# Kernel optimization log

Measured on AMD Instinct MI355X. Metric: run time of the kernel, lower is better.

Reference implementation:

```python
import jax, jax.numpy as jnp
import numpy as np

N, B, D = 4, 256, 128  # agents, batch, latent dim; hidden = 2*D


def setup_inputs() -> dict:
    key = jax.random.key(0)
    k1, k2, k3, k4, k5 = jax.random.split(key, 5)
    z_all = jax.random.normal(k1, (N, B, D), dtype=jnp.float32)
    # per-agent MLP params, stacked over agents; torch Linear layout [out, in]
    W1 = jax.random.normal(k2, (N, 2 * D, D), dtype=jnp.float32) * 0.08
    b1 = jax.random.normal(k3, (N, 2 * D), dtype=jnp.float32) * 0.05
    W2 = jax.random.normal(k4, (N, 1, 2 * D), dtype=jnp.float32) * 0.06
    b2 = jax.random.normal(k5, (N, 1), dtype=jnp.float32) * 0.05
    return {"z_all": z_all, "W1": W1, "b1": b1, "W2": W2, "b2": b2}


def _value(z, W1i, b1i, W2i, b2i):
    # V_i(z): Linear(D,2D) -> tanh -> Linear(2D,1), squeezed to scalar
    h = jnp.tanh(W1i @ z + b1i)          # [2D]
    return jnp.dot(W2i[0], h) + b2i[0]   # scalar


def _pair_hessian(zb, W1i, b1i, W2i, b2i):
    # Hessian of V_i w.r.t. z, batched over B -> [B, D, D]
    hess = jax.hessian(lambda z: _value(z, W1i, b1i, W2i, b2i))
    return jax.vmap(hess)(zb)


def reference(z_all, W1, b1, W2, b2):
    Bn, Dn = z_all.shape[1], z_all.shape[2]
    zero = jnp.zeros((Bn, Dn, Dn), dtype=z_all.dtype)
    rows = []
    for i in range(N):
        cols = []
        for j in range(N):
            if i == j:
                cols.append(zero)
            else:
                cols.append(_pair_hessian(z_all[j], W1[i], b1[i], W2[i], b2[i]))
        rows.append(jnp.stack(cols, axis=0))
    return jnp.stack(rows, axis=0)  # [N, N, B, D, D]
```

## Files before the change

### kernel.cpp

```cpp
#include <hip/hip_runtime.h>
#include <hip/hip_bf16.h>

#define NA 4
#define BB 256
#define DDm 128
#define KKm 256

typedef __attribute__((ext_vector_type(4))) float f32x4;
typedef __attribute__((ext_vector_type(4))) unsigned int u32x4;
typedef __attribute__((ext_vector_type(8))) short bf16x8;

__device__ __forceinline__ unsigned int f2bf(float f) {
  unsigned int bits = __builtin_bit_cast(unsigned int, f);
  unsigned int lsb = (bits >> 16) & 1u;
  return (bits + 0x7fffu + lsb) >> 16;
}

__device__ __forceinline__ int swz_off(int a, int k2bytes) {
  return ((a << 9) + k2bytes) ^ ((a & 7) << 4);
}

__global__ __launch_bounds__(256) void prep_kernel(const float* __restrict__ W1,
                                                   unsigned short* __restrict__ Wt_g,
                                                   float* __restrict__ W1T) {
  int blk = blockIdx.x;
  int i = blk >> 3;
  int chunk = blk & 7;
  const float* W1i = W1 + i * KKm * DDm;
  char* Wti = (char*)(Wt_g + i * 32768);
  float* W1Ti = W1T + i * DDm * KKm;
  int base = chunk * 4096;
  for (int idx = base + threadIdx.x; idx < base + 4096; idx += 256) {
    int a = idx >> 8;
    int k = idx & 255;
    float v = W1i[k * DDm + a];
    W1Ti[a * KKm + k] = v;
    *(unsigned short*)(Wti + swz_off(a, k << 1)) = (unsigned short)f2bf(v);
  }
}

__global__ __launch_bounds__(256, 2) void hess_kernel(
    const float* __restrict__ z_all, const float* __restrict__ b1,
    const float* __restrict__ W2, const unsigned short* __restrict__ Wt_g,
    const float* __restrict__ W1T, float* __restrict__ out) {
  __shared__ __align__(16) unsigned short Wt[32768];
  __shared__ __align__(16) float s_lds[8][KKm];

  int t = threadIdx.x;
  int blk = blockIdx.x;
  int pair = blk >> 5;
  int bgrp = blk & 31;
  int i = pair >> 2;
  int j = pair & 3;

  if (i == j) {
    f32x4* zp = (f32x4*)(out + (((size_t)pair * BB + bgrp * 8) << 14));
    f32x4 z4 = (f32x4){0.f, 0.f, 0.f, 0.f};
#pragma unroll
    for (int q = 0; q < 128; ++q) zp[q * 256 + t] = z4;
    return;
  }

  {
    int wv = t >> 6, lane = t & 63;
    const char* src = (const char*)(Wt_g + i * 32768);
#pragma unroll
    for (int it = 0; it < 16; ++it) {
      int off = (it * 4 + wv) * 1024;
      __builtin_amdgcn_global_load_lds(
          (const __attribute__((address_space(1))) unsigned int*)(src + off + lane * 16),
          (__attribute__((address_space(3))) unsigned int*)((char*)Wt + off),
          16, 0, 0);
    }
  }

  {
    const float* w = W1T + i * DDm * KKm + t;
    const float* zj = z_all + ((size_t)j * BB + bgrp * 8) * DDm;
    float ub = b1[i * KKm + t];
    float u[8];
#pragma unroll
    for (int v = 0; v < 8; ++v) u[v] = ub;
#pragma unroll 4
    for (int a = 0; a < DDm; ++a) {
      float wa = w[a * KKm];
#pragma unroll
      for (int v = 0; v < 8; ++v) u[v] = fmaf(wa, zj[v * DDm + a], u[v]);
    }
    float w2v = W2[i * KKm + t];
#pragma unroll
    for (int v = 0; v < 8; ++v) {
      float h = tanhf(u[v]);
      s_lds[v][t] = -2.0f * w2v * h * (1.0f - h * h);
    }
  }
  __syncthreads();

  int wvi = t >> 6, lane = t & 63;
  int g = lane >> 4;
  int lr = lane & 15;
  int bset = wvi >> 1;
  int rb0 = (wvi & 1) * 64;

  f32x4 accA[2][8], accB[2][8];

  auto do_chunk = [&](f32x4 (&acc)[2][8], int rowbase, const float* sb, float* op) {
#pragma unroll
    for (int mt = 0; mt < 2; ++mt)
#pragma unroll
      for (int nt = 0; nt < 8; ++nt) acc[mt][nt] = (f32x4){0.f, 0.f, 0.f, 0.f};

    for (int kc = 0; kc < 8; ++kc) {
      int kbyte = kc * 64 + g * 16;
      const f32x4* sp = (const f32x4*)&sb[kc * 32 + g * 8];
      f32x4 sA = sp[0], sB = sp[1];
      float sv[8] = {sA[0], sA[1], sA[2], sA[3], sB[0], sB[1], sB[2], sB[3]};

      bf16x8 afr[2];
#pragma unroll
      for (int mt = 0; mt < 2; ++mt) {
        int row = rowbase + mt * 16 + lr;
        u32x4 wq = *(const u32x4*)((const char*)Wt + swz_off(row, kbyte));
        u32x4 aq;
#pragma unroll
        for (int q = 0; q < 4; ++q) {
          float lo = __builtin_bit_cast(float, wq[q] << 16) * sv[2 * q];
          float hi = __builtin_bit_cast(float, wq[q] & 0xffff0000u) * sv[2 * q + 1];
          unsigned int lb = __builtin_bit_cast(unsigned short, (__bf16)lo);
          unsigned int hb = __builtin_bit_cast(unsigned short, (__bf16)hi);
          aq[q] = lb | (hb << 16);
        }
        afr[mt] = __builtin_bit_cast(bf16x8, aq);
      }

#pragma unroll
      for (int nt = 0; nt < 8; ++nt) {
        int row = nt * 16 + lr;
        bf16x8 bfr = __builtin_bit_cast(
            bf16x8, *(const u32x4*)((const char*)Wt + swz_off(row, kbyte)));
        acc[0][nt] = __builtin_amdgcn_mfma_f32_16x16x32_bf16(afr[0], bfr, acc[0][nt], 0, 0, 0);
        acc[1][nt] = __builtin_amdgcn_mfma_f32_16x16x32_bf16(afr[1], bfr, acc[1][nt], 0, 0, 0);
      }
    }

#pragma unroll
    for (int mt = 0; mt < 2; ++mt) {
      int rbase = rowbase + mt * 16 + g * 4;
#pragma unroll
      for (int nt = 0; nt < 8; ++nt) {
        int col = nt * 16 + lr;
#pragma unroll
        for (int q = 0; q < 4; ++q) op[(size_t)(rbase + q) * DDm + col] = acc[mt][nt][q];
      }
    }
  };

  for (int bb = 0; bb < 4; ++bb) {
    int bloc = bset * 4 + bb;
    const float* sb = &s_lds[bloc][0];
    float* op = out + (((size_t)pair * BB + bgrp * 8 + bloc) << 14);
    do_chunk(accA, rb0, sb, op);
    do_chunk(accB, rb0 + 32, sb, op);
  }
}

extern "C" void kernel_launch(void* const* d_in, const int* in_sizes, int n_in,
                              void* d_out, int out_size, void* d_ws, size_t ws_size,
                              hipStream_t stream) {
  const float* z_all = (const float*)d_in[0];
  const float* W1 = (const float*)d_in[1];
  const float* b1 = (const float*)d_in[2];
  const float* W2 = (const float*)d_in[3];
  float* out = (float*)d_out;

  unsigned short* Wt_g = (unsigned short*)d_ws;
  float* W1T = (float*)((char*)d_ws + 262144);

  prep_kernel<<<32, 256, 0, stream>>>(W1, Wt_g, W1T);
  hess_kernel<<<16 * 32, 256, 0, stream>>>(z_all, b1, W2, Wt_g, W1T, out);
}
```

Baseline: 69.12 us.

## Overlap previous chunk's global stores with current chunk's MFMA loop

Software-pipelines the Hessian output writes. The stores of the previous 32-row accumulator set are interleaved into the k-loop of the next chunk, and the k-loop is fully unrolled, so global write traffic overlaps with MFMA and LDS work instead of being serialized after each chunk. Keeping two live accumulator sets adds register pressure, and stores are spread one column tile per k-step.

```diff
diff --git a/kernel.cpp b/kernel.cpp
--- a/kernel.cpp
+++ b/kernel.cpp
@@ -100,16 +100,19 @@
   int g = lane >> 4;
   int lr = lane & 15;
   int bset = wvi >> 1;
-  int rb0 = (wvi & 1) * 64;
+  int m0 = (wvi & 1) * 64;
 
   f32x4 accA[2][8], accB[2][8];
 
-  auto do_chunk = [&](f32x4 (&acc)[2][8], int rowbase, const float* sb, float* op) {
+  auto run_chunk = [&](f32x4 (&acc)[2][8], int rowbase, const float* sb,
+                       bool hasPrev, f32x4 (&pacc)[2][8], int prowbase,
+                       float* pop) {
 #pragma unroll
     for (int mt = 0; mt < 2; ++mt)
 #pragma unroll
       for (int nt = 0; nt < 8; ++nt) acc[mt][nt] = (f32x4){0.f, 0.f, 0.f, 0.f};
 
+#pragma unroll
     for (int kc = 0; kc < 8; ++kc) {
       int kbyte = kc * 64 + g * 16;
       const f32x4* sp = (const f32x4*)&sb[kc * 32 + g * 8];
@@ -141,26 +144,42 @@
         acc[0][nt] = __builtin_amdgcn_mfma_f32_16x16x32_bf16(afr[0], bfr, acc[0][nt], 0, 0, 0);
         acc[1][nt] = __builtin_amdgcn_mfma_f32_16x16x32_bf16(afr[1], bfr, acc[1][nt], 0, 0, 0);
       }
-    }
-
-#pragma unroll
-    for (int mt = 0; mt < 2; ++mt) {
-      int rbase = rowbase + mt * 16 + g * 4;
-#pragma unroll
-      for (int nt = 0; nt < 8; ++nt) {
+
+      if (hasPrev) {
+#pragma unroll
+        for (int mt = 0; mt < 2; ++mt) {
+          int rbase = prowbase + mt * 16 + g * 4;
+          int col = kc * 16 + lr;
+#pragma unroll
+          for (int q = 0; q < 4; ++q)
+            pop[(size_t)(rbase + q) * DDm + col] = pacc[mt][kc][q];
+        }
+      }
+    }
+  };
+
+  {
+    const float* sb = &s_lds[bset * 4][0];
+    float* op_prev = out + (((size_t)pair * BB + bgrp * 8 + bset * 4) << 14);
+    run_chunk(accA, m0, sb, false, accB, m0 + 32, op_prev);
+    run_chunk(accB, m0 + 32, sb, true, accA, m0, op_prev);
+    for (int bb = 1; bb < 4; ++bb) {
+      const float* sbb = &s_lds[bset * 4 + bb][0];
+      float* op = out + (((size_t)pair * BB + bgrp * 8 + bset * 4 + bb) << 14);
+      run_chunk(accA, m0, sbb, true, accB, m0 + 32, op_prev);
+      run_chunk(accB, m0 + 32, sbb, true, accA, m0, op);
+      op_prev = op;
+    }
+#pragma unroll
+    for (int nt = 0; nt < 8; ++nt)
+#pragma unroll
+      for (int mt = 0; mt < 2; ++mt) {
+        int rbase = m0 + 32 + mt * 16 + g * 4;
         int col = nt * 16 + lr;
 #pragma unroll
-        for (int q = 0; q < 4; ++q) op[(size_t)(rbase + q) * DDm + col] = acc[mt][nt][q];
-      }
-    }
-  };
-
-  for (int bb = 0; bb < 4; ++bb) {
-    int bloc = bset * 4 + bb;
-    const float* sb = &s_lds[bloc][0];
-    float* op = out + (((size_t)pair * BB + bgrp * 8 + bloc) << 14);
-    do_chunk(accA, rb0, sb, op);
-    do_chunk(accB, rb0 + 32, sb, op);
+        for (int q = 0; q < 4; ++q)
+          op_prev[(size_t)(rbase + q) * DDm + col] = accB[mt][nt][q];
+      }
   }
 }
 
```

After: 117.6 us. 1.7x slower.

## Spread diagonal zero-fill across all blocks and launch only off-diagonal pair blocks

Applied to the files above, without the earlier changes.

Diagonal (i==j) blocks used to sit idle after writing zeros, which unbalanced the grid. The grid now covers only the 12 off-diagonal pairs, with 64 blocks per pair and 4 batch items per block, one per wave. Each block also zero-fills an equal slice of the four diagonal output regions. This balances store bandwidth across the whole GPU, at the cost of more blocks each reloading the W tile into LDS.

```diff
diff --git a/kernel.cpp b/kernel.cpp
--- a/kernel.cpp
+++ b/kernel.cpp
@@ -44,22 +44,15 @@
     const float* __restrict__ W2, const unsigned short* __restrict__ Wt_g,
     const float* __restrict__ W1T, float* __restrict__ out) {
   __shared__ __align__(16) unsigned short Wt[32768];
-  __shared__ __align__(16) float s_lds[8][KKm];
+  __shared__ __align__(16) float s_lds[4][KKm];
 
   int t = threadIdx.x;
   int blk = blockIdx.x;
-  int pair = blk >> 5;
-  int bgrp = blk & 31;
-  int i = pair >> 2;
-  int j = pair & 3;
-
-  if (i == j) {
-    f32x4* zp = (f32x4*)(out + (((size_t)pair * BB + bgrp * 8) << 14));
-    f32x4 z4 = (f32x4){0.f, 0.f, 0.f, 0.f};
-#pragma unroll
-    for (int q = 0; q < 128; ++q) zp[q * 256 + t] = z4;
-    return;
-  }
+  int pair = blk >> 6;
+  int bgrp = blk & 63;
+  int i = pair / 3;
+  int rr = pair - i * 3;
+  int j = rr + (rr >= i ? 1 : 0);
 
   {
     int wv = t >> 6, lane = t & 63;
@@ -75,21 +68,34 @@
   }
 
   {
+    f32x4 z4 = (f32x4){0.f, 0.f, 0.f, 0.f};
+    int start = blk * 5462;
+    int end = start + 5462;
+    if (end > 4194304) end = 4194304;
+    f32x4* ov = (f32x4*)out;
+    for (int dv = start + t; dv < end; dv += 256) {
+      int p = dv >> 20;
+      int r = dv & 1048575;
+      ov[(size_t)p * 5242880 + r] = z4;
+    }
+  }
+
+  {
     const float* w = W1T + i * DDm * KKm + t;
-    const float* zj = z_all + ((size_t)j * BB + bgrp * 8) * DDm;
+    const float* zj = z_all + ((size_t)j * BB + bgrp * 4) * DDm;
     float ub = b1[i * KKm + t];
-    float u[8];
+    float u[4];
 #pragma unroll
-    for (int v = 0; v < 8; ++v) u[v] = ub;
+    for (int v = 0; v < 4; ++v) u[v] = ub;
 #pragma unroll 4
     for (int a = 0; a < DDm; ++a) {
       float wa = w[a * KKm];
 #pragma unroll
-      for (int v = 0; v < 8; ++v) u[v] = fmaf(wa, zj[v * DDm + a], u[v]);
+      for (int v = 0; v < 4; ++v) u[v] = fmaf(wa, zj[v * DDm + a], u[v]);
     }
     float w2v = W2[i * KKm + t];
 #pragma unroll
-    for (int v = 0; v < 8; ++v) {
+    for (int v = 0; v < 4; ++v) {
       float h = tanhf(u[v]);
       s_lds[v][t] = -2.0f * w2v * h * (1.0f - h * h);
     }
@@ -99,8 +105,6 @@
   int wvi = t >> 6, lane = t & 63;
   int g = lane >> 4;
   int lr = lane & 15;
-  int bset = wvi >> 1;
-  int rb0 = (wvi & 1) * 64;
 
   f32x4 accA[2][8], accB[2][8];
 
@@ -155,12 +159,14 @@
     }
   };
 
-  for (int bb = 0; bb < 4; ++bb) {
-    int bloc = bset * 4 + bb;
-    const float* sb = &s_lds[bloc][0];
-    float* op = out + (((size_t)pair * BB + bgrp * 8 + bloc) << 14);
-    do_chunk(accA, rb0, sb, op);
-    do_chunk(accB, rb0 + 32, sb, op);
+  {
+    const float* sb = &s_lds[wvi][0];
+    size_t pid = (size_t)(i * NA + j);
+    float* op = out + ((pid * BB + bgrp * 4 + wvi) << 14);
+    do_chunk(accA, 0, sb, op);
+    do_chunk(accB, 32, sb, op);
+    do_chunk(accA, 64, sb, op);
+    do_chunk(accB, 96, sb, op);
   }
 }
 
@@ -177,5 +183,5 @@
   float* W1T = (float*)((char*)d_ws + 262144);
 
   prep_kernel<<<32, 256, 0, stream>>>(W1, Wt_g, W1T);
-  hess_kernel<<<16 * 32, 256, 0, stream>>>(z_all, b1, W2, Wt_g, W1T, out);
+  hess_kernel<<<768, 256, 0, stream>>>(z_all, b1, W2, Wt_g, W1T, out);
 }
```

New measurement: 72.96 us. 1.06x slower.
